# Kernel optimization log

Measured on AMD Instinct MI355X. Metric: run time of the kernel, lower is better.

Reference implementation:

```python
import jax, jax.numpy as jnp
import numpy as np

B, C, P, N_PARTS, JOINTS_PER_PART = 2048, 256, 15, 5, 3
GROUPS = 4
EPS = 1e-5
MASK_VAL = 10000.0


def setup_inputs() -> dict:
    key = jax.random.key(0)
    k1, k2, k3 = jax.random.split(key, 3)
    g = (2 * C) // GROUPS  # 128
    return {
        "x": jax.random.normal(k1, (B, C, P, 1), jnp.float32),
        "conv_w": jax.random.normal(k2, (GROUPS, g, g), jnp.float32) * 0.05,
        "conv_b": jax.random.normal(k3, (2 * C,), jnp.float32) * 0.05,
        "bn_gamma": jnp.ones((2 * C,), jnp.float32),
        "bn_beta": jnp.zeros((2 * C,), jnp.float32),
    }


def reference(x, conv_w, conv_b, bn_gamma, bn_beta):
    Bb, Cc, Pp, _ = x.shape
    xs = x[..., 0]  # [B, C, P]

    # relative[b,c,i,k] = xs[b,c,k] - xs[b,c,i]; for a row i in part p the
    # reduction is max_k(relative - MASK_VAL * [k in part p]). Since the mask
    # only depends on the part of row i, precompute the per-part masked max of
    # xs over k and broadcast-subtract xs[i].
    part_id = jnp.arange(Pp) // JOINTS_PER_PART  # [P]
    Mg = jnp.where(part_id[None, :] == jnp.arange(N_PARTS)[:, None], -MASK_VAL, 0.0)  # [5, P]
    m = jnp.max(xs[:, :, None, :] + Mg[None, None, :, :], axis=-1)  # [B, C, 5]
    tmp = m[:, :, part_id] - xs  # [B, C, P]

    y = jnp.concatenate([xs, tmp], axis=1)  # [B, 2C, P]

    # grouped 1x1 conv (groups=4)
    g = (2 * Cc) // GROUPS
    y4 = y.reshape(Bb, GROUPS, g, Pp)
    z = jnp.einsum('bgip,goi->bgop', y4, conv_w).reshape(Bb, 2 * Cc, Pp)
    z = z + conv_b[None, :, None]

    # BatchNorm2d, training mode: biased batch stats over (B, spatial)
    mean = jnp.mean(z, axis=(0, 2))
    var = jnp.var(z, axis=(0, 2))
    zn = (z - mean[None, :, None]) * jax.lax.rsqrt(var + EPS)[None, :, None]
    out = jax.nn.relu(zn * bn_gamma[None, :, None] + bn_beta[None, :, None])
    return out[..., None]  # [B, 2C, P, 1]
```

## Files before the change

kernel.cpp:

```cpp
#include <hip/hip_runtime.h>
#include <hip/hip_bf16.h>
#include <cstdint>

#define EPS_ 1e-5f
#define NVALID_F 30720.0f

typedef __bf16 bf16x8 __attribute__((ext_vector_type(8)));
typedef float f32x16 __attribute__((ext_vector_type(16)));
typedef float f32x4 __attribute__((ext_vector_type(4)));
typedef unsigned short u16x8 __attribute__((ext_vector_type(8)));

__device__ __forceinline__ unsigned short f2bf(float f) {
  unsigned u = __float_as_uint(f);
  u += 0x7FFFu + ((u >> 16) & 1u);
  return (unsigned short)(u >> 16);
}
__device__ __forceinline__ float bf2f(unsigned short h) {
  return __uint_as_float((unsigned)h << 16);
}

__global__ void k_wprep(const float* __restrict__ w, unsigned short* __restrict__ wf) {
  int q = blockIdx.x * 256 + threadIdx.x;
  int l = q & 63, ks = (q >> 6) & 7, mt = (q >> 9) & 3, g = q >> 11;
  int o = mt * 32 + (l & 31);
  int i = ks * 16 + (l >> 5) * 8;
  const float* src = w + ((size_t)(g * 128 + o) * 128 + i);
  u16x8 v;
#pragma unroll
  for (int j = 0; j < 8; ++j) v[j] = f2bf(src[j]);
  *(u16x8*)(wf + (size_t)q * 8) = v;
}

__device__ __forceinline__ void build_Y_union(const float* __restrict__ x, int b0, int t,
                                              unsigned short* __restrict__ Yt) {
  {
    const f32x4* src = (const f32x4*)(x + (size_t)b0 * 3840);
    f32x4* dst = (f32x4*)Yt;
    for (int q = t; q < 1920; q += 256) dst[q] = src[q];
  }
  __syncthreads();
  float v[2][15];
  const float* xsf = (const float*)Yt;
#pragma unroll
  for (int bi = 0; bi < 2; ++bi)
#pragma unroll
    for (int p = 0; p < 15; ++p) v[bi][p] = xsf[bi * 3840 + t * 15 + p];
  __syncthreads();
#pragma unroll
  for (int bi = 0; bi < 2; ++bi) {
    float pm[5];
#pragma unroll
    for (int q = 0; q < 5; ++q)
      pm[q] = fmaxf(fmaxf(v[bi][3 * q], v[bi][3 * q + 1]), v[bi][3 * q + 2]);
    float mq[5];
    mq[0] = fmaxf(fmaxf(pm[1], pm[2]), fmaxf(pm[3], pm[4]));
    mq[1] = fmaxf(fmaxf(pm[0], pm[2]), fmaxf(pm[3], pm[4]));
    mq[2] = fmaxf(fmaxf(pm[0], pm[1]), fmaxf(pm[3], pm[4]));
    mq[3] = fmaxf(fmaxf(pm[0], pm[1]), fmaxf(pm[2], pm[4]));
    mq[4] = fmaxf(fmaxf(pm[0], pm[1]), fmaxf(pm[2], pm[3]));
    const int c0 = bi * 16;
#pragma unroll
    for (int p = 0; p < 15; ++p) {
      Yt[(c0 + p) * 520 + t] = f2bf(v[bi][p]);
      Yt[(c0 + p) * 520 + 256 + t] = f2bf(mq[p / 3] - v[bi][p]);
    }
    Yt[(c0 + 15) * 520 + t] = 0;
    Yt[(c0 + 15) * 520 + 256 + t] = 0;
  }
}

__global__ __launch_bounds__(256, 4) void k_pass1(const float* __restrict__ x,
                                                  const unsigned short* __restrict__ wf,
                                                  float2* __restrict__ Part) {
  __shared__ __align__(16) unsigned short Yt[32 * 520];
  const int t = threadIdx.x;
  const int b0 = blockIdx.x * 2;
  build_Y_union(x, b0, t, Yt);
  __syncthreads();

  const int lane = t & 63, g = t >> 6;
  const int l31 = lane & 31, lh = lane >> 5;
  const bf16x8* Wfv = (const bf16x8*)wf;

  bf16x8 bfr[8];
  const unsigned short* yrow = &Yt[l31 * 520 + g * 128 + lh * 8];
#pragma unroll
  for (int ks = 0; ks < 8; ++ks)
    bfr[ks] = *(const bf16x8*)(yrow + ks * 16);

  for (int mt = 0; mt < 4; ++mt) {
    bf16x8 wr[8];
#pragma unroll
    for (int ks = 0; ks < 8; ++ks)
      wr[ks] = Wfv[(size_t)((g * 4 + mt) * 8 + ks) * 64 + lane];
    f32x16 acc;
#pragma unroll
    for (int r = 0; r < 16; ++r) acc[r] = 0.f;
#pragma unroll
    for (int ks = 0; ks < 8; ++ks)
      acc = __builtin_amdgcn_mfma_f32_32x32x16_bf16(bfr[ks], wr[ks], acc, 0, 0, 0);
    float s = 0.f, s2 = 0.f;
#pragma unroll
    for (int r = 0; r < 16; ++r) { float vv = acc[r]; s += vv; s2 = fmaf(vv, vv, s2); }
    s += __shfl_xor(s, 32, 64);
    s2 += __shfl_xor(s2, 32, 64);
    const int ch = g * 128 + mt * 32 + l31;
    if (lane < 32) Part[(size_t)blockIdx.x * 512 + ch] = make_float2(s, s2);
  }
}

__global__ void k_stats(const float2* __restrict__ Part,
                        const float* __restrict__ gamma, const float* __restrict__ beta,
                        float2* __restrict__ AB) {
  const int t = threadIdx.x;
  const int chb = blockIdx.x * 8;
  const int c = t & 7, r0 = t >> 3;
  float s = 0.f, s2 = 0.f;
  for (int k = 0; k < 32; ++k) {
    float2 vv = Part[(size_t)(r0 + 32 * k) * 512 + chb + c];
    s += vv.x; s2 += vv.y;
  }
  s += __shfl_xor(s, 8, 64);  s2 += __shfl_xor(s2, 8, 64);
  s += __shfl_xor(s, 16, 64); s2 += __shfl_xor(s2, 16, 64);
  s += __shfl_xor(s, 32, 64); s2 += __shfl_xor(s2, 32, 64);
  __shared__ float2 red[4][8];
  if ((t & 63) < 8) red[t >> 6][c] = make_float2(s, s2);
  __syncthreads();
  if (t < 8) {
    float S = 0.f, S2 = 0.f;
#pragma unroll
    for (int w = 0; w < 4; ++w) { S += red[w][t].x; S2 += red[w][t].y; }
    const float inv = 1.f / NVALID_F;
    float mean = S * inv;
    float var = fmaxf(S2 * inv - mean * mean, 0.f);
    float a = gamma[chb + t] * rsqrtf(var + EPS_);
    AB[chb + t] = make_float2(a, beta[chb + t] - mean * a);
  }
}

__global__ __launch_bounds__(256, 4) void k_pass2(const float* __restrict__ x,
                                                  const unsigned short* __restrict__ wf,
                                                  const float2* __restrict__ AB,
                                                  float* __restrict__ out) {
  __shared__ __align__(16) unsigned short Yt[32 * 520];
  __shared__ float aArr[512], bArr[512];
  const int t = threadIdx.x;
  const int b0 = blockIdx.x * 2;

#pragma unroll
  for (int i = 0; i < 2; ++i) {
    int ch = i * 256 + t;
    float2 ab = AB[ch];
    aArr[ch] = ab.x; bArr[ch] = ab.y;
  }
  build_Y_union(x, b0, t, Yt);
  __syncthreads();

  {
    const int lane = t & 63, g = t >> 6;
    const int l31 = lane & 31, lh = lane >> 5;
    const bf16x8* Wfv = (const bf16x8*)wf;

    bf16x8 bfr[8];
    const unsigned short* yrow = &Yt[l31 * 520 + g * 128 + lh * 8];
#pragma unroll
    for (int ks = 0; ks < 8; ++ks)
      bfr[ks] = *(const bf16x8*)(yrow + ks * 16);

    for (int mt = 0; mt < 4; ++mt) {
      bf16x8 wr[8];
#pragma unroll
      for (int ks = 0; ks < 8; ++ks)
        wr[ks] = Wfv[(size_t)((g * 4 + mt) * 8 + ks) * 64 + lane];
      f32x16 acc;
#pragma unroll
      for (int r = 0; r < 16; ++r) acc[r] = 0.f;
#pragma unroll
      for (int ks = 0; ks < 8; ++ks)
        acc = __builtin_amdgcn_mfma_f32_32x32x16_bf16(bfr[ks], wr[ks], acc, 0, 0, 0);
      const int ch = g * 128 + mt * 32 + l31;
#pragma unroll
      for (int r = 0; r < 16; ++r) {
        int row = (r & 3) + 8 * (r >> 2) + 4 * lh;
        Yt[row * 520 + ch] = f2bf(acc[r]);
      }
    }
  }
  __syncthreads();

#pragma unroll
  for (int bi = 0; bi < 2; ++bi) {
    float2* slab = (float2*)(out + (size_t)(b0 + bi) * 7680);
#pragma unroll 5
    for (int k = 0; k < 15; ++k) {
      int e0 = k * 512 + 2 * t;
      int ch0 = e0 / 15, p0 = e0 - ch0 * 15;
      int e1 = e0 + 1;
      int ch1 = e1 / 15, p1 = e1 - ch1 * 15;
      float f0 = bf2f(Yt[(bi * 16 + p0) * 520 + ch0]);
      float f1 = bf2f(Yt[(bi * 16 + p1) * 520 + ch1]);
      slab[k * 256 + t] = make_float2(
          fmaxf(fmaf(f0, aArr[ch0], bArr[ch0]), 0.f),
          fmaxf(fmaf(f1, aArr[ch1], bArr[ch1]), 0.f));
    }
  }
}

extern "C" void kernel_launch(void* const* d_in, const int* in_sizes, int n_in,
                              void* d_out, int out_size, void* d_ws, size_t ws_size,
                              hipStream_t stream) {
  const float* x = (const float*)d_in[0];
  const float* cw = (const float*)d_in[1];
  const float* gamma = (const float*)d_in[3];
  const float* beta = (const float*)d_in[4];

  unsigned short* wf = (unsigned short*)d_ws;
  float2* Part = (float2*)(wf + 65536);
  float2* AB = Part + (size_t)1024 * 512;

  hipLaunchKernelGGL(k_wprep, dim3(32), dim3(256), 0, stream, cw, wf);
  hipLaunchKernelGGL(k_pass1, dim3(1024), dim3(256), 0, stream, x, wf, Part);
  hipLaunchKernelGGL(k_stats, dim3(64), dim3(256), 0, stream, Part, gamma, beta, AB);
  hipLaunchKernelGGL(k_pass2, dim3(1024), dim3(256), 0, stream, x, wf, AB, (float*)d_out);
}
```

Before: 48.27 us.

## Fuse pass1, stats and pass2 into one cooperative kernel with grid syncs

Replaces the three-kernel pipeline (conv+stats, stats reduction, recompute conv+normalize) with a single cooperative kernel of 512 blocks, each handling 4 batch items. Conv results stay in LDS across two grid.sync barriers, so x is read only once and the second matmul pass is dropped. The costs are a larger LDS footprint (about 70KB per block, limiting occupancy to 2 blocks per CU), two grid-wide barriers, and reliance on cooperative launch, with the old three-kernel path kept as a fallback.

```diff
diff --git a/kernel.cpp b/kernel.cpp
--- a/kernel.cpp
+++ b/kernel.cpp
@@ -1,9 +1,12 @@
 #include <hip/hip_runtime.h>
 #include <hip/hip_bf16.h>
+#include <hip/hip_cooperative_groups.h>
 #include <cstdint>
 
 #define EPS_ 1e-5f
 #define NVALID_F 30720.0f
+
+namespace cg = cooperative_groups;
 
 typedef __bf16 bf16x8 __attribute__((ext_vector_type(8)));
 typedef float f32x16 __attribute__((ext_vector_type(16)));
@@ -29,6 +32,158 @@
 #pragma unroll
   for (int j = 0; j < 8; ++j) v[j] = f2bf(src[j]);
   *(u16x8*)(wf + (size_t)q * 8) = v;
+}
+
+__global__ __launch_bounds__(256, 2) void k_coop2(const float* __restrict__ x,
+                                                  const unsigned short* __restrict__ wf,
+                                                  float2* __restrict__ Part,
+                                                  const float* __restrict__ gamma,
+                                                  const float* __restrict__ beta,
+                                                  float2* __restrict__ AB,
+                                                  float* __restrict__ out) {
+  __shared__ __align__(16) unsigned short Yt[64 * 520];
+  __shared__ float aArr[512], bArr[512];
+  __shared__ float2 red[4][8];
+  cg::grid_group grid = cg::this_grid();
+  const int t = threadIdx.x;
+  const int bid = blockIdx.x;
+  const int b0 = bid * 4;
+
+  {
+    const f32x4* src = (const f32x4*)(x + (size_t)b0 * 3840);
+    f32x4* dst = (f32x4*)Yt;
+    for (int q = t; q < 3840; q += 256) dst[q] = src[q];
+  }
+  __syncthreads();
+  float v[4][15];
+  {
+    const float* xsf = (const float*)Yt;
+#pragma unroll
+    for (int bi = 0; bi < 4; ++bi)
+#pragma unroll
+      for (int p = 0; p < 15; ++p) v[bi][p] = xsf[bi * 3840 + t * 15 + p];
+  }
+  __syncthreads();
+#pragma unroll
+  for (int bi = 0; bi < 4; ++bi) {
+    float pm[5];
+#pragma unroll
+    for (int q = 0; q < 5; ++q)
+      pm[q] = fmaxf(fmaxf(v[bi][3 * q], v[bi][3 * q + 1]), v[bi][3 * q + 2]);
+    float mq[5];
+    mq[0] = fmaxf(fmaxf(pm[1], pm[2]), fmaxf(pm[3], pm[4]));
+    mq[1] = fmaxf(fmaxf(pm[0], pm[2]), fmaxf(pm[3], pm[4]));
+    mq[2] = fmaxf(fmaxf(pm[0], pm[1]), fmaxf(pm[3], pm[4]));
+    mq[3] = fmaxf(fmaxf(pm[0], pm[1]), fmaxf(pm[2], pm[4]));
+    mq[4] = fmaxf(fmaxf(pm[0], pm[1]), fmaxf(pm[2], pm[3]));
+    const int c0 = bi * 16;
+#pragma unroll
+    for (int p = 0; p < 15; ++p) {
+      Yt[(c0 + p) * 520 + t] = f2bf(v[bi][p]);
+      Yt[(c0 + p) * 520 + 256 + t] = f2bf(mq[p / 3] - v[bi][p]);
+    }
+    Yt[(c0 + 15) * 520 + t] = 0;
+    Yt[(c0 + 15) * 520 + 256 + t] = 0;
+  }
+  __syncthreads();
+
+  {
+    const int lane = t & 63, g = t >> 6;
+    const int l31 = lane & 31, lh = lane >> 5;
+    const bf16x8* Wfv = (const bf16x8*)wf;
+
+    bf16x8 bfr0[8], bfr1[8];
+    const unsigned short* yr0 = &Yt[l31 * 520 + g * 128 + lh * 8];
+    const unsigned short* yr1 = &Yt[(32 + l31) * 520 + g * 128 + lh * 8];
+#pragma unroll
+    for (int ks = 0; ks < 8; ++ks) {
+      bfr0[ks] = *(const bf16x8*)(yr0 + ks * 16);
+      bfr1[ks] = *(const bf16x8*)(yr1 + ks * 16);
+    }
+    for (int mt = 0; mt < 4; ++mt) {
+      bf16x8 wr[8];
+#pragma unroll
+      for (int ks = 0; ks < 8; ++ks)
+        wr[ks] = Wfv[(size_t)((g * 4 + mt) * 8 + ks) * 64 + lane];
+      f32x16 a0, a1;
+#pragma unroll
+      for (int r = 0; r < 16; ++r) { a0[r] = 0.f; a1[r] = 0.f; }
+#pragma unroll
+      for (int ks = 0; ks < 8; ++ks) {
+        a0 = __builtin_amdgcn_mfma_f32_32x32x16_bf16(bfr0[ks], wr[ks], a0, 0, 0, 0);
+        a1 = __builtin_amdgcn_mfma_f32_32x32x16_bf16(bfr1[ks], wr[ks], a1, 0, 0, 0);
+      }
+      float s = 0.f, s2 = 0.f;
+#pragma unroll
+      for (int r = 0; r < 16; ++r) {
+        float v0 = a0[r], v1 = a1[r];
+        s += v0 + v1; s2 = fmaf(v0, v0, fmaf(v1, v1, s2));
+      }
+      s += __shfl_xor(s, 32, 64);
+      s2 += __shfl_xor(s2, 32, 64);
+      const int ch = g * 128 + mt * 32 + l31;
+      if (lane < 32) Part[(size_t)bid * 512 + ch] = make_float2(s, s2);
+#pragma unroll
+      for (int r = 0; r < 16; ++r) {
+        int row = (r & 3) + 8 * (r >> 2) + 4 * lh;
+        Yt[row * 520 + ch] = f2bf(a0[r]);
+        Yt[(32 + row) * 520 + ch] = f2bf(a1[r]);
+      }
+    }
+  }
+
+  grid.sync();
+
+  if (bid < 64) {
+    const int chb = bid * 8;
+    const int c = t & 7, r0 = t >> 3;
+    float s = 0.f, s2 = 0.f;
+    for (int k = 0; k < 16; ++k) {
+      float2 vv = Part[(size_t)(r0 + 32 * k) * 512 + chb + c];
+      s += vv.x; s2 += vv.y;
+    }
+    s += __shfl_xor(s, 8, 64);  s2 += __shfl_xor(s2, 8, 64);
+    s += __shfl_xor(s, 16, 64); s2 += __shfl_xor(s2, 16, 64);
+    s += __shfl_xor(s, 32, 64); s2 += __shfl_xor(s2, 32, 64);
+    if ((t & 63) < 8) red[t >> 6][c] = make_float2(s, s2);
+    __syncthreads();
+    if (t < 8) {
+      float S = 0.f, S2 = 0.f;
+#pragma unroll
+      for (int w = 0; w < 4; ++w) { S += red[w][t].x; S2 += red[w][t].y; }
+      const float inv = 1.f / NVALID_F;
+      float mean = S * inv;
+      float var = fmaxf(S2 * inv - mean * mean, 0.f);
+      float a = gamma[chb + t] * rsqrtf(var + EPS_);
+      AB[chb + t] = make_float2(a, beta[chb + t] - mean * a);
+    }
+  }
+
+  grid.sync();
+
+#pragma unroll
+  for (int i = 0; i < 2; ++i) {
+    int ch = i * 256 + t;
+    float2 ab = AB[ch];
+    aArr[ch] = ab.x; bArr[ch] = ab.y;
+  }
+  __syncthreads();
+#pragma unroll
+  for (int bi = 0; bi < 4; ++bi) {
+    float2* slab = (float2*)(out + (size_t)(b0 + bi) * 7680);
+#pragma unroll 5
+    for (int k = 0; k < 15; ++k) {
+      int e0 = k * 512 + 2 * t;
+      int ch0 = e0 / 15, p0 = e0 - ch0 * 15;
+      int e1 = e0 + 1;
+      int ch1 = e1 / 15, p1 = e1 - ch1 * 15;
+      float f0 = bf2f(Yt[(bi * 16 + p0) * 520 + ch0]);
+      float f1 = bf2f(Yt[(bi * 16 + p1) * 520 + ch1]);
+      slab[k * 256 + t] = make_float2(
+          fmaxf(fmaf(f0, aArr[ch0], bArr[ch0]), 0.f),
+          fmaxf(fmaf(f1, aArr[ch1], bArr[ch1]), 0.f));
+    }
+  }
 }
 
 __device__ __forceinline__ void build_Y_union(const float* __restrict__ x, int b0, int t,
@@ -217,9 +372,17 @@
   unsigned short* wf = (unsigned short*)d_ws;
   float2* Part = (float2*)(wf + 65536);
   float2* AB = Part + (size_t)1024 * 512;
+  float* outf = (float*)d_out;
 
   hipLaunchKernelGGL(k_wprep, dim3(32), dim3(256), 0, stream, cw, wf);
-  hipLaunchKernelGGL(k_pass1, dim3(1024), dim3(256), 0, stream, x, wf, Part);
-  hipLaunchKernelGGL(k_stats, dim3(64), dim3(256), 0, stream, Part, gamma, beta, AB);
-  hipLaunchKernelGGL(k_pass2, dim3(1024), dim3(256), 0, stream, x, wf, AB, (float*)d_out);
-}
+
+  void* args[] = {(void*)&x, (void*)&wf, (void*)&Part, (void*)&gamma,
+                  (void*)&beta, (void*)&AB, (void*)&outf};
+  hipError_t cerr = hipLaunchCooperativeKernel((const void*)k_coop2, dim3(512),
+                                               dim3(256), args, 0, stream);
+  if (cerr != hipSuccess) {
+    hipLaunchKernelGGL(k_pass1, dim3(1024), dim3(256), 0, stream, x, wf, Part);
+    hipLaunchKernelGGL(k_stats, dim3(64), dim3(256), 0, stream, Part, gamma, beta, AB);
+    hipLaunchKernelGGL(k_pass2, dim3(1024), dim3(256), 0, stream, x, wf, AB, outf);
+  }
+}
```

After: 151.7 us. 214% more time.

## Process one batch per block with half-padded MFMA tiles and more occupancy

Applied to the files above, without the earlier changes.

Each block now handles one batch element instead of two, doubling the grid to 2048 blocks and halving LDS per block. Launch bounds rise to allow 8 blocks per CU. The 32-row MFMA tile now carries only 16 valid rows, with the upper half zeroed, so half of the matrix-core work is wasted. Pass2 now reads the BN scale and shift directly from global memory instead of staging them in LDS. The change trades doubled weight fragment loads and MFMA work per sample for more parallelism and occupancy.

```diff
diff --git a/kernel.cpp b/kernel.cpp
--- a/kernel.cpp
+++ b/kernel.cpp
@@ -31,62 +31,62 @@
   *(u16x8*)(wf + (size_t)q * 8) = v;
 }
 
-__device__ __forceinline__ void build_Y_union(const float* __restrict__ x, int b0, int t,
-                                              unsigned short* __restrict__ Yt) {
+__device__ __forceinline__ void build_Y1(const float* __restrict__ x, int b, int t,
+                                         unsigned short* __restrict__ Yt) {
   {
-    const f32x4* src = (const f32x4*)(x + (size_t)b0 * 3840);
+    const f32x4* src = (const f32x4*)(x + (size_t)b * 3840);
     f32x4* dst = (f32x4*)Yt;
-    for (int q = t; q < 1920; q += 256) dst[q] = src[q];
-  }
-  __syncthreads();
-  float v[2][15];
-  const float* xsf = (const float*)Yt;
-#pragma unroll
-  for (int bi = 0; bi < 2; ++bi)
-#pragma unroll
-    for (int p = 0; p < 15; ++p) v[bi][p] = xsf[bi * 3840 + t * 15 + p];
-  __syncthreads();
-#pragma unroll
-  for (int bi = 0; bi < 2; ++bi) {
-    float pm[5];
-#pragma unroll
-    for (int q = 0; q < 5; ++q)
-      pm[q] = fmaxf(fmaxf(v[bi][3 * q], v[bi][3 * q + 1]), v[bi][3 * q + 2]);
-    float mq[5];
-    mq[0] = fmaxf(fmaxf(pm[1], pm[2]), fmaxf(pm[3], pm[4]));
-    mq[1] = fmaxf(fmaxf(pm[0], pm[2]), fmaxf(pm[3], pm[4]));
-    mq[2] = fmaxf(fmaxf(pm[0], pm[1]), fmaxf(pm[3], pm[4]));
-    mq[3] = fmaxf(fmaxf(pm[0], pm[1]), fmaxf(pm[2], pm[4]));
-    mq[4] = fmaxf(fmaxf(pm[0], pm[1]), fmaxf(pm[2], pm[3]));
-    const int c0 = bi * 16;
-#pragma unroll
-    for (int p = 0; p < 15; ++p) {
-      Yt[(c0 + p) * 520 + t] = f2bf(v[bi][p]);
-      Yt[(c0 + p) * 520 + 256 + t] = f2bf(mq[p / 3] - v[bi][p]);
-    }
-    Yt[(c0 + 15) * 520 + t] = 0;
-    Yt[(c0 + 15) * 520 + 256 + t] = 0;
-  }
-}
-
-__global__ __launch_bounds__(256, 4) void k_pass1(const float* __restrict__ x,
+    for (int q = t; q < 960; q += 256) dst[q] = src[q];
+  }
+  __syncthreads();
+  float v[15];
+  {
+    const float* xsf = (const float*)Yt;
+#pragma unroll
+    for (int p = 0; p < 15; ++p) v[p] = xsf[t * 15 + p];
+  }
+  __syncthreads();
+  float pm[5];
+#pragma unroll
+  for (int q = 0; q < 5; ++q) pm[q] = fmaxf(fmaxf(v[3 * q], v[3 * q + 1]), v[3 * q + 2]);
+  float mq[5];
+  mq[0] = fmaxf(fmaxf(pm[1], pm[2]), fmaxf(pm[3], pm[4]));
+  mq[1] = fmaxf(fmaxf(pm[0], pm[2]), fmaxf(pm[3], pm[4]));
+  mq[2] = fmaxf(fmaxf(pm[0], pm[1]), fmaxf(pm[3], pm[4]));
+  mq[3] = fmaxf(fmaxf(pm[0], pm[1]), fmaxf(pm[2], pm[4]));
+  mq[4] = fmaxf(fmaxf(pm[0], pm[1]), fmaxf(pm[2], pm[3]));
+#pragma unroll
+  for (int p = 0; p < 15; ++p) {
+    Yt[p * 520 + t] = f2bf(v[p]);
+    Yt[p * 520 + 256 + t] = f2bf(mq[p / 3] - v[p]);
+  }
+  Yt[15 * 520 + t] = 0;
+  Yt[15 * 520 + 256 + t] = 0;
+}
+
+__global__ __launch_bounds__(256, 8) void k_pass1(const float* __restrict__ x,
                                                   const unsigned short* __restrict__ wf,
                                                   float2* __restrict__ Part) {
-  __shared__ __align__(16) unsigned short Yt[32 * 520];
+  __shared__ __align__(16) unsigned short Yt[16 * 520];
   const int t = threadIdx.x;
-  const int b0 = blockIdx.x * 2;
-  build_Y_union(x, b0, t, Yt);
+  build_Y1(x, blockIdx.x, t, Yt);
   __syncthreads();
 
   const int lane = t & 63, g = t >> 6;
   const int l31 = lane & 31, lh = lane >> 5;
   const bf16x8* Wfv = (const bf16x8*)wf;
 
+  union ZU { u16x8 u; bf16x8 b; };
+  ZU zz; zz.u = (u16x8){0, 0, 0, 0, 0, 0, 0, 0};
+  const bf16x8 zero8 = zz.b;
+
   bf16x8 bfr[8];
-  const unsigned short* yrow = &Yt[l31 * 520 + g * 128 + lh * 8];
-#pragma unroll
-  for (int ks = 0; ks < 8; ++ks)
-    bfr[ks] = *(const bf16x8*)(yrow + ks * 16);
+  const unsigned short* yrow = &Yt[(l31 & 15) * 520 + g * 128 + lh * 8];
+#pragma unroll
+  for (int ks = 0; ks < 8; ++ks) {
+    bf16x8 ld = *(const bf16x8*)(yrow + ks * 16);
+    bfr[ks] = (l31 < 16) ? ld : zero8;
+  }
 
   for (int mt = 0; mt < 4; ++mt) {
     bf16x8 wr[8];
@@ -116,7 +116,7 @@
   const int chb = blockIdx.x * 8;
   const int c = t & 7, r0 = t >> 3;
   float s = 0.f, s2 = 0.f;
-  for (int k = 0; k < 32; ++k) {
+  for (int k = 0; k < 64; ++k) {
     float2 vv = Part[(size_t)(r0 + 32 * k) * 512 + chb + c];
     s += vv.x; s2 += vv.y;
   }
@@ -138,22 +138,13 @@
   }
 }
 
-__global__ __launch_bounds__(256, 4) void k_pass2(const float* __restrict__ x,
+__global__ __launch_bounds__(256, 8) void k_pass2(const float* __restrict__ x,
                                                   const unsigned short* __restrict__ wf,
                                                   const float2* __restrict__ AB,
                                                   float* __restrict__ out) {
-  __shared__ __align__(16) unsigned short Yt[32 * 520];
-  __shared__ float aArr[512], bArr[512];
+  __shared__ __align__(16) unsigned short Yt[16 * 520];
   const int t = threadIdx.x;
-  const int b0 = blockIdx.x * 2;
-
-#pragma unroll
-  for (int i = 0; i < 2; ++i) {
-    int ch = i * 256 + t;
-    float2 ab = AB[ch];
-    aArr[ch] = ab.x; bArr[ch] = ab.y;
-  }
-  build_Y_union(x, b0, t, Yt);
+  build_Y1(x, blockIdx.x, t, Yt);
   __syncthreads();
 
   {
@@ -161,11 +152,17 @@
     const int l31 = lane & 31, lh = lane >> 5;
     const bf16x8* Wfv = (const bf16x8*)wf;
 
+    union ZU { u16x8 u; bf16x8 b; };
+    ZU zz; zz.u = (u16x8){0, 0, 0, 0, 0, 0, 0, 0};
+    const bf16x8 zero8 = zz.b;
+
     bf16x8 bfr[8];
-    const unsigned short* yrow = &Yt[l31 * 520 + g * 128 + lh * 8];
-#pragma unroll
-    for (int ks = 0; ks < 8; ++ks)
-      bfr[ks] = *(const bf16x8*)(yrow + ks * 16);
+    const unsigned short* yrow = &Yt[(l31 & 15) * 520 + g * 128 + lh * 8];
+#pragma unroll
+    for (int ks = 0; ks < 8; ++ks) {
+      bf16x8 ld = *(const bf16x8*)(yrow + ks * 16);
+      bfr[ks] = (l31 < 16) ? ld : zero8;
+    }
 
     for (int mt = 0; mt < 4; ++mt) {
       bf16x8 wr[8];
@@ -182,27 +179,26 @@
 #pragma unroll
       for (int r = 0; r < 16; ++r) {
         int row = (r & 3) + 8 * (r >> 2) + 4 * lh;
-        Yt[row * 520 + ch] = f2bf(acc[r]);
+        if (row < 16) Yt[row * 520 + ch] = f2bf(acc[r]);
       }
     }
   }
   __syncthreads();
 
-#pragma unroll
-  for (int bi = 0; bi < 2; ++bi) {
-    float2* slab = (float2*)(out + (size_t)(b0 + bi) * 7680);
+  float2* slab = (float2*)(out + (size_t)blockIdx.x * 7680);
 #pragma unroll 5
-    for (int k = 0; k < 15; ++k) {
-      int e0 = k * 512 + 2 * t;
-      int ch0 = e0 / 15, p0 = e0 - ch0 * 15;
-      int e1 = e0 + 1;
-      int ch1 = e1 / 15, p1 = e1 - ch1 * 15;
-      float f0 = bf2f(Yt[(bi * 16 + p0) * 520 + ch0]);
-      float f1 = bf2f(Yt[(bi * 16 + p1) * 520 + ch1]);
-      slab[k * 256 + t] = make_float2(
-          fmaxf(fmaf(f0, aArr[ch0], bArr[ch0]), 0.f),
-          fmaxf(fmaf(f1, aArr[ch1], bArr[ch1]), 0.f));
-    }
+  for (int k = 0; k < 15; ++k) {
+    int e0 = k * 512 + 2 * t;
+    int ch0 = e0 / 15, p0 = e0 - ch0 * 15;
+    int e1 = e0 + 1;
+    int ch1 = e1 / 15, p1 = e1 - ch1 * 15;
+    float2 ab0 = AB[ch0];
+    float2 ab1 = AB[ch1];
+    float f0 = bf2f(Yt[p0 * 520 + ch0]);
+    float f1 = bf2f(Yt[p1 * 520 + ch1]);
+    slab[k * 256 + t] = make_float2(
+        fmaxf(fmaf(f0, ab0.x, ab0.y), 0.f),
+        fmaxf(fmaf(f1, ab1.x, ab1.y), 0.f));
   }
 }
 
@@ -216,10 +212,10 @@
 
   unsigned short* wf = (unsigned short*)d_ws;
   float2* Part = (float2*)(wf + 65536);
-  float2* AB = Part + (size_t)1024 * 512;
+  float2* AB = Part + (size_t)2048 * 512;
 
   hipLaunchKernelGGL(k_wprep, dim3(32), dim3(256), 0, stream, cw, wf);
-  hipLaunchKernelGGL(k_pass1, dim3(1024), dim3(256), 0, stream, x, wf, Part);
+  hipLaunchKernelGGL(k_pass1, dim3(2048), dim3(256), 0, stream, x, wf, Part);
   hipLaunchKernelGGL(k_stats, dim3(64), dim3(256), 0, stream, Part, gamma, beta, AB);
-  hipLaunchKernelGGL(k_pass2, dim3(1024), dim3(256), 0, stream, x, wf, AB, (float*)d_out);
-}
+  hipLaunchKernelGGL(k_pass2, dim3(2048), dim3(256), 0, stream, x, wf, AB, (float*)d_out);
+}
```

New measurement: 92.81 us. +92.3%, slower.

## Fuse BN stats reduction into pass1 via atomic counter; widen pass2 stores

Applied to the files above, without the earlier changes.

Removes the separate k_stats launch. Each pass1 block takes a rank from a global atomic counter. The last 64 blocks spin until all 1024 blocks have published their partials, then each reduces one 8-channel slice into AB. The counter is reset in k_wprep. Pass2's output loop now writes float4 instead of float2. This saves a kernel launch gap, but the late blocks spin-wait, which assumes all earlier blocks can make progress while they wait.

```diff
diff --git a/kernel.cpp b/kernel.cpp
--- a/kernel.cpp
+++ b/kernel.cpp
@@ -19,7 +19,9 @@
   return __uint_as_float((unsigned)h << 16);
 }
 
-__global__ void k_wprep(const float* __restrict__ w, unsigned short* __restrict__ wf) {
+__global__ void k_wprep(const float* __restrict__ w, unsigned short* __restrict__ wf,
+                        int* __restrict__ ctr) {
+  if (blockIdx.x == 0 && threadIdx.x == 0) *ctr = 0;
   int q = blockIdx.x * 256 + threadIdx.x;
   int l = q & 63, ks = (q >> 6) & 7, mt = (q >> 9) & 3, g = q >> 11;
   int o = mt * 32 + (l & 31);
@@ -71,7 +73,11 @@
 
 __global__ __launch_bounds__(256, 4) void k_pass1(const float* __restrict__ x,
                                                   const unsigned short* __restrict__ wf,
-                                                  float2* __restrict__ Part) {
+                                                  float2* __restrict__ Part,
+                                                  const float* __restrict__ gamma,
+                                                  const float* __restrict__ beta,
+                                                  float2* __restrict__ AB,
+                                                  int* __restrict__ ctr) {
   __shared__ __align__(16) unsigned short Yt[32 * 520];
   const int t = threadIdx.x;
   const int b0 = blockIdx.x * 2;
@@ -107,13 +113,23 @@
     const int ch = g * 128 + mt * 32 + l31;
     if (lane < 32) Part[(size_t)blockIdx.x * 512 + ch] = make_float2(s, s2);
   }
-}
-
-__global__ void k_stats(const float2* __restrict__ Part,
-                        const float* __restrict__ gamma, const float* __restrict__ beta,
-                        float2* __restrict__ AB) {
-  const int t = threadIdx.x;
-  const int chb = blockIdx.x * 8;
+
+  __threadfence();
+  __shared__ int rank_s;
+  if (t == 0)
+    rank_s = atomicAdd(ctr, 1);
+  __syncthreads();
+  const int rank = rank_s;
+  if (rank < 960) return;
+
+  if (t == 0) {
+    while (__hip_atomic_load(ctr, __ATOMIC_ACQUIRE, __HIP_MEMORY_SCOPE_AGENT) < 1024)
+      __builtin_amdgcn_s_sleep(16);
+  }
+  __syncthreads();
+  __threadfence();
+
+  const int chb = (rank - 960) * 8;
   const int c = t & 7, r0 = t >> 3;
   float s = 0.f, s2 = 0.f;
   for (int k = 0; k < 32; ++k) {
@@ -123,13 +139,13 @@
   s += __shfl_xor(s, 8, 64);  s2 += __shfl_xor(s2, 8, 64);
   s += __shfl_xor(s, 16, 64); s2 += __shfl_xor(s2, 16, 64);
   s += __shfl_xor(s, 32, 64); s2 += __shfl_xor(s2, 32, 64);
-  __shared__ float2 red[4][8];
-  if ((t & 63) < 8) red[t >> 6][c] = make_float2(s, s2);
+  float2* red = (float2*)Yt;
+  if ((t & 63) < 8) red[(t >> 6) * 8 + c] = make_float2(s, s2);
   __syncthreads();
   if (t < 8) {
     float S = 0.f, S2 = 0.f;
 #pragma unroll
-    for (int w = 0; w < 4; ++w) { S += red[w][t].x; S2 += red[w][t].y; }
+    for (int w = 0; w < 4; ++w) { S += red[w * 8 + t].x; S2 += red[w * 8 + t].y; }
     const float inv = 1.f / NVALID_F;
     float mean = S * inv;
     float var = fmaxf(S2 * inv - mean * mean, 0.f);
@@ -188,21 +204,22 @@
   }
   __syncthreads();
 
-#pragma unroll
-  for (int bi = 0; bi < 2; ++bi) {
-    float2* slab = (float2*)(out + (size_t)(b0 + bi) * 7680);
+  f32x4* slab4 = (f32x4*)(out + (size_t)b0 * 7680);
 #pragma unroll 5
-    for (int k = 0; k < 15; ++k) {
-      int e0 = k * 512 + 2 * t;
-      int ch0 = e0 / 15, p0 = e0 - ch0 * 15;
-      int e1 = e0 + 1;
-      int ch1 = e1 / 15, p1 = e1 - ch1 * 15;
-      float f0 = bf2f(Yt[(bi * 16 + p0) * 520 + ch0]);
-      float f1 = bf2f(Yt[(bi * 16 + p1) * 520 + ch1]);
-      slab[k * 256 + t] = make_float2(
-          fmaxf(fmaf(f0, aArr[ch0], bArr[ch0]), 0.f),
-          fmaxf(fmaf(f1, aArr[ch1], bArr[ch1]), 0.f));
+  for (int it = 0; it < 15; ++it) {
+    int q = it * 256 + t;
+    int e = q * 4;
+    int bi = e >= 7680;
+    int rbase = e - bi * 7680;
+    f32x4 o;
+#pragma unroll
+    for (int j = 0; j < 4; ++j) {
+      int r = rbase + j;
+      int ch = r / 15, p = r - ch * 15;
+      float f = bf2f(Yt[(bi * 16 + p) * 520 + ch]);
+      o[j] = fmaxf(fmaf(f, aArr[ch], bArr[ch]), 0.f);
     }
+    slab4[q] = o;
   }
 }
 
@@ -217,9 +234,10 @@
   unsigned short* wf = (unsigned short*)d_ws;
   float2* Part = (float2*)(wf + 65536);
   float2* AB = Part + (size_t)1024 * 512;
-
-  hipLaunchKernelGGL(k_wprep, dim3(32), dim3(256), 0, stream, cw, wf);
-  hipLaunchKernelGGL(k_pass1, dim3(1024), dim3(256), 0, stream, x, wf, Part);
-  hipLaunchKernelGGL(k_stats, dim3(64), dim3(256), 0, stream, Part, gamma, beta, AB);
+  int* ctr = (int*)(AB + 512);
+
+  hipLaunchKernelGGL(k_wprep, dim3(32), dim3(256), 0, stream, cw, wf, ctr);
+  hipLaunchKernelGGL(k_pass1, dim3(1024), dim3(256), 0, stream, x, wf, Part,
+                     gamma, beta, AB, ctr);
   hipLaunchKernelGGL(k_pass2, dim3(1024), dim3(256), 0, stream, x, wf, AB, (float*)d_out);
 }
```

Result: slower. 127.7 us (+164.6%).
